# Kernel tuning notes

Hardware: AMD Instinct MI355X
Metric: run time of the kernel (lower is better)

The kernel has to match this reference:

```python
import jax, jax.numpy as jnp
import numpy as np

DIM = 384
NH = 6
HD = DIM // NH  # 64
WS = (6, 12)    # window_size (dilated_size=[1,1] so total_window_size == window_size)
SS = (3, 6)     # shift_size
N = WS[0] * WS[1]  # 72 tokens per window


def _make_mask(H, W):
    # Faithful replication of SD_attn.create_mask (static, so computed in numpy).
    wh, ww = WS
    sh, sw = SS
    img = np.zeros((H, W), np.float32)
    cnt = 0
    for hs in (slice(0, -wh), slice(-wh, -sh), slice(-sh, None)):
        for wsl in (slice(0, -ww), slice(-ww, 0), slice(0, None)):
            img[hs, wsl] = cnt
            cnt += 1
    # window partition -> (nW, N)
    m = img.reshape(H // wh, wh, W // ww, ww).transpose(0, 2, 1, 3).reshape(-1, wh * ww)
    d = m[:, None, :] - m[:, :, None]  # (nW, N, N), [i,j] = m[j]-m[i]
    return np.where(d != 0, -np.inf, 0.0).astype(np.float32)


def _rope2d(x):
    # 2D axial rotary embedding over the (wh, ww) window grid.
    # x: (M, wh, ww, hd); first half of pair-channels rotated by h-position, second half by w-position.
    wh, ww, hd = x.shape[1], x.shape[2], x.shape[3]
    half = hd // 2
    inv = 1.0 / (10000.0 ** (np.arange(0, half, 2, dtype=np.float32) / half))  # (half//2,)
    ah = np.arange(wh, dtype=np.float32)[:, None] * inv  # (wh, half//2)
    aw = np.arange(ww, dtype=np.float32)[:, None] * inv  # (ww, half//2)
    ang = np.concatenate([
        np.broadcast_to(ah[:, None, :], (wh, ww, half // 2)),
        np.broadcast_to(aw[None, :, :], (wh, ww, half // 2)),
    ], -1)  # (wh, ww, half)
    cos = jnp.asarray(np.cos(ang), dtype=x.dtype)
    sin = jnp.asarray(np.sin(ang), dtype=x.dtype)
    x1, x2 = x[..., 0::2], x[..., 1::2]
    return jnp.stack([x1 * cos - x2 * sin, x1 * sin + x2 * cos], -1).reshape(x.shape)


def setup_inputs() -> dict:
    key = jax.random.key(0)
    ks = jax.random.split(key, 5)
    x = jax.random.normal(ks[0], (2, 192, 384, DIM), jnp.float32)
    w_qkv = 0.02 * jax.random.normal(ks[1], (3 * DIM, DIM), jnp.float32)
    b_qkv = 0.02 * jax.random.normal(ks[2], (3 * DIM,), jnp.float32)
    w_proj = 0.02 * jax.random.normal(ks[3], (DIM, DIM), jnp.float32)
    b_proj = 0.02 * jax.random.normal(ks[4], (DIM,), jnp.float32)
    return {"x": x, "w_qkv": w_qkv, "b_qkv": b_qkv, "w_proj": w_proj, "b_proj": b_proj}


def reference(x, w_qkv, b_qkv, w_proj, b_proj):
    B, H, W, C = x.shape
    wh, ww = WS
    sh, sw = SS
    nH, nWc = H // wh, W // ww
    nwin = nH * nWc
    B_ = B * nwin
    scale = HD ** -0.5

    # cyclic shift + window partition (dilated_size=[1,1] => plain swin windows)
    xs = jnp.roll(x, (-sh, -sw), axis=(1, 2))
    xw = xs.reshape(B, nH, wh, nWc, ww, C).transpose(0, 1, 3, 2, 4, 5).reshape(B_, N, C)

    qkv = (xw @ w_qkv.T + b_qkv).reshape(B_, N, 3, NH, HD).transpose(2, 0, 3, 1, 4)
    q, k, v = qkv[0], qkv[1], qkv[2]  # (B_, NH, N, HD)

    q = _rope2d(q.reshape(-1, wh, ww, HD)).reshape(B_, NH, N, HD)
    k = _rope2d(k.reshape(-1, wh, ww, HD)).reshape(B_, NH, N, HD)

    attn = jnp.einsum('bhnd,bhmd->bhnm', q * scale, k)  # (B_, NH, N, N)
    mask = jnp.asarray(_make_mask(H, W))                 # (nwin, N, N)
    attn = (attn.reshape(B, nwin, NH, N, N) + mask[None, :, None]).reshape(B_, NH, N, N)
    attn = jax.nn.softmax(attn, axis=-1)
    save_attn = attn.mean(axis=1)  # mean over heads -> (B_, N, N)

    out = jnp.einsum('bhnm,bhmd->bhnd', attn, v).transpose(0, 2, 1, 3).reshape(B_, N, C)
    out = out.reshape(B, nH, nWc, wh, ww, C).transpose(0, 1, 3, 2, 4, 5).reshape(B, H, W, C)
    out = jnp.roll(out, (sh, sw), axis=(1, 2))
    out = out @ w_proj.T + b_proj
    return out, save_attn
```

## Files before the change

### kernel.cpp

```cpp
#include <hip/hip_runtime.h>

typedef __attribute__((ext_vector_type(8))) __bf16 bf16x8;
typedef __attribute__((ext_vector_type(4))) float f32x4;
typedef unsigned short u16;
typedef unsigned int u32;

__device__ __forceinline__ u16 f2bf(float x){
  u32 u = __float_as_uint(x);
  return (u16)((u + 0x7fffu + ((u >> 16) & 1u)) >> 16);
}
__device__ __forceinline__ u32 pkbf(float lo, float hi){
  u32 r; asm("v_cvt_pk_bf16_f32 %0, %1, %2" : "=v"(r) : "v"(lo), "v"(hi)); return r;
}

union FragU { uint4 u4; bf16x8 bf; };

__device__ __forceinline__ bf16x8 lds_frag(const unsigned char* smem, int off, int row, int strideB, int kElem){
  int byte = (row * strideB + kElem * 2) ^ ((row & 7) << 4);
  FragU f; f.u4 = *reinterpret_cast<const uint4*>(smem + off + byte);
  return f.bf;
}

typedef __attribute__((address_space(3))) unsigned char lds_u8;
typedef __attribute__((address_space(1))) const unsigned char g_u8;
__device__ __forceinline__ void glds16(const void* g, void* l){
  __builtin_amdgcn_global_load_lds((g_u8*)g, (lds_u8*)l, 16, 0, 0);
}

__global__ void prep_weights(const float* __restrict__ wq, const float* __restrict__ wp,
                             u16* __restrict__ wqb, u16* __restrict__ wpb){
  int i = blockIdx.x * 256 + threadIdx.x;
  wqb[i] = f2bf(wq[i]);
  if (i < 147456) wpb[i] = f2bf(wp[i]);
}

__global__ void prep_x(const float* __restrict__ x, u16* __restrict__ xb){
  size_t i = ((size_t)blockIdx.x * 256 + threadIdx.x) * 8;
  float4 f0 = *reinterpret_cast<const float4*>(x + i);
  float4 f1 = *reinterpret_cast<const float4*>(x + i + 4);
  uint4 q;
  q.x = pkbf(f0.x, f0.y); q.y = pkbf(f0.z, f0.w);
  q.z = pkbf(f1.x, f1.y); q.w = pkbf(f1.z, f1.w);
  *reinterpret_cast<uint4*>(xb + i) = q;
}

#define WA_OFF 0
#define WB_OFF 10240
#define WVT    0
#define WTC    61440
#define WTS    62592
__launch_bounds__(256, 2)
__global__ void qkv_win(const u16* __restrict__ xb, const u16* __restrict__ wqb,
                        const float* __restrict__ bq, float* __restrict__ out,
                        u16* __restrict__ vws)
{
  __shared__ __align__(16) unsigned char smem[63744];
  const int tid  = threadIdx.x;
  const int wc   = tid >> 6;
  const int lane = tid & 63;
  const int l15  = lane & 15;
  const int lhi  = lane >> 4;

  const int bid = blockIdx.x;
  const int l   = (bid & 7) * 768 + (bid >> 3);
  const int g   = l / 3;
  const int sec = l - g * 3;
  const int bIdx = g >> 10;
  const int win  = g & 1023;
  const int wi   = win >> 5;
  const int wj   = win & 31;

  auto rowof = [&](int t)->size_t {
    int r = t / 12, c = t - r * 12;
    int hh = wi * 6 + r + 3;  if (hh >= 192) hh -= 192;
    int ww = wj * 12 + c + 6; if (ww >= 384) ww -= 384;
    return ((size_t)bIdx * 192 + hh) * 384 + ww;
  };

  float* tabc = reinterpret_cast<float*>(smem + WTC);
  float* tabs = reinterpret_cast<float*>(smem + WTS);
  for (int i = tid; i < 288; i += 256){
    int pos = i >> 4, m = i & 15;
    float pv = (pos < 6) ? (float)pos : (float)(pos - 6);
    float ang = pv * __expf(-(float)m * 0.5756462732485114f);
    tabc[i] = cosf(ang);
    tabs[i] = sinf(ang);
  }

  size_t arow[3]; int asoff[3]; bool aval[3];
  #pragma unroll
  for (int it = 0; it < 3; ++it){
    int c = it * 256 + tid;
    aval[it] = (it < 2) || (tid < 128);
    int t = c >> 3, p = c & 7;
    int tc = (t < 72) ? t : 71;
    arow[it]  = rowof(tc);
    asoff[it] = ((p ^ (t & 7)) << 3);
  }

  f32x4 acc[5][6];
  #pragma unroll
  for (int mt = 0; mt < 5; ++mt)
    #pragma unroll
    for (int nt = 0; nt < 6; ++nt) acc[mt][nt] = 0.0f;

  for (int kk = 0; kk < 6; ++kk){
    #pragma unroll
    for (int it = 0; it < 3; ++it){
      if (aval[it])
        glds16(xb + arow[it] * 384 + kk * 64 + asoff[it],
               smem + WA_OFF + (it * 256 + tid) * 16);
    }
    #pragma unroll
    for (int it = 0; it < 12; ++it){
      int c = it * 256 + tid;
      int n = c >> 3, p = c & 7;
      glds16(wqb + (size_t)(sec * 384 + n) * 384 + kk * 64 + ((p ^ (n & 7)) << 3),
             smem + WB_OFF + c * 16);
    }
    __syncthreads();
    #pragma unroll
    for (int ks = 0; ks < 2; ++ks){
      const int kEl = ks * 32 + lhi * 8;
      bf16x8 af[5], bfr[6];
      #pragma unroll
      for (int mt = 0; mt < 5; ++mt)
        af[mt] = lds_frag(smem, WA_OFF, mt * 16 + l15, 128, kEl);
      #pragma unroll
      for (int nt = 0; nt < 6; ++nt)
        bfr[nt] = lds_frag(smem, WB_OFF, wc * 96 + nt * 16 + l15, 128, kEl);
      __builtin_amdgcn_s_setprio(1);
      #pragma unroll
      for (int mt = 0; mt < 5; ++mt)
        #pragma unroll
        for (int nt = 0; nt < 6; ++nt)
          acc[mt][nt] = __builtin_amdgcn_mfma_f32_16x16x32_bf16(af[mt], bfr[nt], acc[mt][nt], 0, 0, 0);
      __builtin_amdgcn_s_setprio(0);
    }
    __syncthreads();
  }

  if (sec < 2){
    u16* qk = (u16*)out + (sec ? 56623104u : 0u) + (size_t)g * 27648;
    #pragma unroll
    for (int nt = 0; nt < 6; ++nt){
      const int ch  = wc * 96 + nt * 16 + l15;
      const int h   = ch >> 6;
      const int chh = ch & 63;
      const float bias = bq[sec * 384 + ch];
      const int p2  = chh >> 1;
      const int m   = p2 & 15;
      const bool isR = (p2 < 16);
      const bool ev  = ((chh & 1) == 0);
      #pragma unroll
      for (int mt = 0; mt < 5; ++mt){
        #pragma unroll
        for (int r = 0; r < 4; ++r){
          const int tok = mt * 16 + lhi * 4 + r;
          float v = acc[mt][nt][r] + bias;
          float o = __shfl_xor(v, 1);
          int tr = tok / 12;
          int pos = isR ? tr : (6 + tok - tr * 12);
          float cc = tabc[pos * 16 + m], ssn = tabs[pos * 16 + m];
          float nv = ev ? (v * cc - o * ssn) : (o * ssn + v * cc);
          if (sec == 0) nv *= 0.125f;
          if (tok < 72)
            qk[(size_t)h * 4608 + tok * 64 + chh] = f2bf(nv);
        }
      }
    }
  } else {
    #pragma unroll
    for (int nt = 0; nt < 6; ++nt){
      const int ch = wc * 96 + nt * 16 + l15;
      const float bv = bq[768 + ch];
      #pragma unroll
      for (int mt = 0; mt < 5; ++mt){
        const int tok0 = mt * 16 + lhi * 4;
        uint2 pk;
        pk.x = pkbf(acc[mt][nt][0] + bv, acc[mt][nt][1] + bv);
        pk.y = pkbf(acc[mt][nt][2] + bv, acc[mt][nt][3] + bv);
        *reinterpret_cast<uint2*>(smem + WVT + ch * 160 + tok0 * 2) = pk;
      }
    }
    __syncthreads();
    u16* vd = vws + (size_t)g * 30720;
    #pragma unroll
    for (int it = 0; it < 15; ++it){
      int c  = it * 256 + tid;
      int ch = c / 10;
      int p  = c - ch * 10;
      uint4 val;
      if (p == 9){ val.x = 0; val.y = 0; val.z = 0; val.w = 0; }
      else val = *reinterpret_cast<const uint4*>(smem + WVT + c * 16);
      *reinterpret_cast<uint4*>(vd + (size_t)(ch >> 6) * 5120 + (ch & 63) * 80 + p * 8) = val;
    }
  }
}

#define QH4 0
#define KH4 10240
#define VT4 20480
#define SMEM4 30976
__launch_bounds__(320, 5)
__global__ void win_attn6(const u16* __restrict__ qkg,
                          const u16* __restrict__ vws,
                          float* __restrict__ out,
                          u16* __restrict__ axb)
{
  __shared__ __align__(16) unsigned char smem[SMEM4];
  const int tid  = threadIdx.x;
  const int wave = tid >> 6;
  const int lane = tid & 63;
  const int l15  = lane & 15;
  const int lhi  = lane >> 4;

  const int bid  = blockIdx.x;
  const int wgid = (bid & 7) * 256 + (bid >> 3);
  const int bIdx = wgid >> 10;
  const int win  = wgid & 1023;
  const int wi   = win >> 5;
  const int wj   = win & 31;
  const bool maskWin = (wi == 31);
  const int g    = wgid;

  auto rowof = [&](int t)->size_t {
    int r = t / 12, c = t - r * 12;
    int hh = wi * 6 + r + 3;  if (hh >= 192) hh -= 192;
    int ww = wj * 12 + c + 6; if (ww >= 384) ww -= 384;
    return ((size_t)bIdx * 192 + hh) * 384 + ww;
  };
  const int qtok = wave * 16 + l15;
  const bool tv = (qtok < 72);
  const size_t qrow = rowof(tv ? qtok : 71);

  const u16* qsl0 = qkg + (size_t)g * 27648;
  const u16* ksl0 = qkg + 56623104u + (size_t)g * 27648;
  const u16* vsl0 = vws + (size_t)g * 30720;

  if (tid < 64) *reinterpret_cast<u32*>(smem + VT4 + 10240 + tid * 4) = 0u;

  float sv[5][4];
  #pragma unroll
  for (int a2 = 0; a2 < 5; ++a2)
    #pragma unroll
    for (int b2 = 0; b2 < 4; ++b2) sv[a2][b2] = 0.0f;

  for (int h = 0; h < 6; ++h){
    const u16* qsl = qsl0 + h * 4608;
    const u16* ksl = ksl0 + h * 4608;
    const u16* vsl = vsl0 + h * 5120;
    #pragma unroll
    for (int it = 0; it < 2; ++it){
      int c = it * 320 + tid;
      int t = c >> 3, p = c & 7;
      int tc = (t < 72) ? t : 71;
      int s = (p ^ (t & 7)) << 3;
      glds16(qsl + tc * 64 + s, smem + QH4 + c * 16);
      glds16(ksl + tc * 64 + s, smem + KH4 + c * 16);
      glds16(vsl + c * 8,       smem + VT4 + c * 16);
    }
    __syncthreads();

    f32x4 pf[5];
    #pragma unroll
    for (int nt = 0; nt < 5; ++nt) pf[nt] = 0.0f;
    __builtin_amdgcn_s_setprio(1);
    #pragma unroll
    for (int ks = 0; ks < 2; ++ks){
      const int kEl = ks * 32 + lhi * 8;
      bf16x8 qf = lds_frag(smem, QH4, qtok, 128, kEl);
      #pragma unroll
      for (int nt = 0; nt < 5; ++nt){
        bf16x8 kf = lds_frag(smem, KH4, nt * 16 + l15, 128, kEl);
        pf[nt] = __builtin_amdgcn_mfma_f32_16x16x32_bf16(kf, qf, pf[nt], 0, 0, 0);
      }
    }
    __builtin_amdgcn_s_setprio(0);

    float mx = -1e30f;
    #pragma unroll
    for (int nt = 0; nt < 5; ++nt)
      #pragma unroll
      for (int r = 0; r < 4; ++r){
        const int kk2 = nt * 16 + lhi * 4 + r;
        bool valid = (kk2 < 72) && (!maskWin || ((kk2 < 36) == (qtok < 36)));
        float val = valid ? pf[nt][r] : -1e30f;
        pf[nt][r] = val;
        mx = fmaxf(mx, val);
      }
    mx = fmaxf(mx, __shfl_xor(mx, 16));
    mx = fmaxf(mx, __shfl_xor(mx, 32));
    float sm = 0.0f;
    #pragma unroll
    for (int nt = 0; nt < 5; ++nt)
      #pragma unroll
      for (int r = 0; r < 4; ++r){
        float e = __expf(pf[nt][r] - mx);
        pf[nt][r] = e; sm += e;
      }
    sm += __shfl_xor(sm, 16);
    sm += __shfl_xor(sm, 32);
    const float inv = 1.0f / sm;
    u32 pp[5][2];
    #pragma unroll
    for (int nt = 0; nt < 5; ++nt){
      float p0 = pf[nt][0] * inv, p1 = pf[nt][1] * inv;
      float p2 = pf[nt][2] * inv, p3 = pf[nt][3] * inv;
      sv[nt][0] += p0; sv[nt][1] += p1; sv[nt][2] += p2; sv[nt][3] += p3;
      pp[nt][0] = pkbf(p0, p1);
      pp[nt][1] = pkbf(p2, p3);
    }

    f32x4 oacc[4];
    #pragma unroll
    for (int nt = 0; nt < 4; ++nt) oacc[nt] = 0.0f;
    #pragma unroll
    for (int ks = 0; ks < 3; ++ks){
      FragU pb;
      u32 w[4];
      #pragma unroll
      for (int w_ = 0; w_ < 4; ++w_){
        int srcLane = l15 + 16 * ((lane >> 4 & 1) * 2 + (w_ >> 1));
        u32 c0 = __shfl(pp[ks * 2][w_ & 1], srcLane);
        u32 c1 = (ks * 2 + 1 < 5) ? __shfl(pp[ks * 2 + 1][w_ & 1], srcLane) : 0u;
        w[w_] = (lhi & 2) ? c1 : c0;
      }
      pb.u4.x = w[0]; pb.u4.y = w[1]; pb.u4.z = w[2]; pb.u4.w = w[3];
      const int kEl = ks * 32 + lhi * 8;
      __builtin_amdgcn_s_setprio(1);
      #pragma unroll
      for (int nt = 0; nt < 4; ++nt){
        FragU vf;
        vf.u4 = *reinterpret_cast<const uint4*>(smem + VT4 + (nt * 16 + l15) * 160 + kEl * 2);
        oacc[nt] = __builtin_amdgcn_mfma_f32_16x16x32_bf16(vf.bf, pb.bf, oacc[nt], 0, 0, 0);
      }
      __builtin_amdgcn_s_setprio(0);
    }
    if (tv){
      u16* ao = axb + qrow * 384 + h * 64;
      #pragma unroll
      for (int nt = 0; nt < 4; ++nt){
        uint2 pk;
        pk.x = pkbf(oacc[nt][0], oacc[nt][1]);
        pk.y = pkbf(oacc[nt][2], oacc[nt][3]);
        *reinterpret_cast<uint2*>(ao + nt * 16 + lhi * 4) = pk;
      }
    }
    __syncthreads();
  }

  if (tv){
    float* so = out + 56623104ull + (size_t)wgid * 5184 + (size_t)qtok * 72;
    const float c6 = 1.0f / 6.0f;
    #pragma unroll
    for (int nt = 0; nt < 4; ++nt){
      float4 v4; v4.x = sv[nt][0]*c6; v4.y = sv[nt][1]*c6; v4.z = sv[nt][2]*c6; v4.w = sv[nt][3]*c6;
      *reinterpret_cast<float4*>(so + nt * 16 + lhi * 4) = v4;
    }
    if (lhi < 2){
      float4 v4; v4.x = sv[4][0]*c6; v4.y = sv[4][1]*c6; v4.z = sv[4][2]*c6; v4.w = sv[4][3]*c6;
      *reinterpret_cast<float4*>(so + 64 + lhi * 4) = v4;
    }
  }
}

#define B6STR 12288
__launch_bounds__(512, 4)
__global__ void proj_gemm2(const u16* __restrict__ axb,
                           const u16* __restrict__ wpb, const float* __restrict__ bp,
                           float* __restrict__ out)
{
  __shared__ __align__(16) unsigned char smem[24576];
  const int tid  = threadIdx.x;
  const int wave = tid >> 6;
  const int lane = tid & 63;
  const int l15  = lane & 15;
  const int lhi  = lane >> 4;
  const int wr   = wave >> 2;
  const int wc   = wave & 3;
  const size_t row0 = (size_t)blockIdx.x * 128;
  const int ny   = blockIdx.y;

  const u16* bsec = wpb + (size_t)(ny * 192) * 384;
  auto stageB = [&](int t, int bufOff){
    {
      int c = tid, row = c >> 2, ccd = c & 3;
      int ccs = ccd ^ ((row >> 1) & 3);
      glds16(bsec + (size_t)row * 384 + t * 32 + ccs * 8, smem + bufOff + c * 16);
    }
    if (tid < 256){
      int c = 512 + tid, row = c >> 2, ccd = c & 3;
      int ccs = ccd ^ ((row >> 1) & 3);
      glds16(bsec + (size_t)row * 384 + t * 32 + ccs * 8, smem + bufOff + c * 16);
    }
  };

  const u16* abase = axb + (row0 + wr * 64 + l15) * 384 + lhi * 8;

  f32x4 acc[4][3];
  #pragma unroll
  for (int mt = 0; mt < 4; ++mt)
    #pragma unroll
    for (int nt = 0; nt < 3; ++nt) acc[mt][nt] = 0.0f;

  FragU a_cur[4], a_nxt[4];
  #pragma unroll
  for (int mt = 0; mt < 4; ++mt)
    a_cur[mt].u4 = *reinterpret_cast<const uint4*>(abase + mt * 6144);
  stageB(0, 0);
  __syncthreads();

  int buf = 0;
  for (int t = 0; t < 12; ++t){
    if (t < 11){
      stageB(t + 1, buf ^ B6STR);
      #pragma unroll
      for (int mt = 0; mt < 4; ++mt)
        a_nxt[mt].u4 = *reinterpret_cast<const uint4*>(abase + mt * 6144 + (t + 1) * 32);
    }
    FragU bfr[3];
    #pragma unroll
    for (int nt = 0; nt < 3; ++nt){
      int rown = wc * 48 + nt * 16 + l15;
      int byte = buf + rown * 64 + ((lhi ^ ((rown >> 1) & 3)) << 4);
      bfr[nt].u4 = *reinterpret_cast<const uint4*>(smem + byte);
    }
    #pragma unroll
    for (int mt = 0; mt < 4; ++mt)
      #pragma unroll
      for (int nt = 0; nt < 3; ++nt)
        acc[mt][nt] = __builtin_amdgcn_mfma_f32_16x16x32_bf16(a_cur[mt].bf, bfr[nt].bf, acc[mt][nt], 0, 0, 0);
    __syncthreads();
    #pragma unroll
    for (int mt = 0; mt < 4; ++mt) a_cur[mt] = a_nxt[mt];
    buf ^= B6STR;
  }

  float bpv[3];
  #pragma unroll
  for (int nt = 0; nt < 3; ++nt) bpv[nt] = bp[ny * 192 + wc * 48 + nt * 16 + l15];
  #pragma unroll
  for (int mt = 0; mt < 4; ++mt)
    #pragma unroll
    for (int nt = 0; nt < 3; ++nt){
      const int ch = ny * 192 + wc * 48 + nt * 16 + l15;
      #pragma unroll
      for (int r = 0; r < 4; ++r){
        size_t grow = row0 + wr * 64 + mt * 16 + lhi * 4 + r;
        out[grow * 384 + ch] = acc[mt][nt][r] + bpv[nt];
      }
    }
}

extern "C" void kernel_launch(void* const* d_in, const int* in_sizes, int n_in,
                              void* d_out, int out_size, void* d_ws, size_t ws_size,
                              hipStream_t stream)
{
  const float* x  = (const float*)d_in[0];
  const float* wq = (const float*)d_in[1];
  const float* bq = (const float*)d_in[2];
  const float* wp = (const float*)d_in[3];
  const float* bp = (const float*)d_in[4];
  float* out = (float*)d_out;

  u16* wqb = (u16*)d_ws;
  u16* wpb = (u16*)((char*)d_ws + 442368 * 2);
  u16* vws = (u16*)((char*)d_ws + 1179648);
  u16* xb  = (u16*)((char*)d_ws + 127008768);

  prep_weights<<<1728, 256, 0, stream>>>(wq, wp, wqb, wpb);
  prep_x<<<27648, 256, 0, stream>>>(x, xb);
  qkv_win<<<6144, 256, 0, stream>>>(xb, wqb, bq, out, vws);
  win_attn6<<<2048, 320, 0, stream>>>((const u16*)out, vws, out, xb);
  proj_gemm2<<<dim3(1152, 2), 512, 0, stream>>>(xb, wpb, bp, out);
}
```

Before: 636.3 us.

## Process two windows per QKV block to share weight tiles; swizzle proj grid

The QKV GEMM kernel now uses 512-thread blocks that each handle two adjacent windows. The staged weight tile is shared across both, which halves weight traffic per window and halves the block count. The V writeback is serialized per window through LDS with extra barriers. The projection GEMM switches to a 1D grid with an XCD-aware remap so blocks sharing the same weight half and rows land on the same chiplet. The larger LDS footprint may limit occupancy.

```diff
diff --git a/kernel.cpp b/kernel.cpp
--- a/kernel.cpp
+++ b/kernel.cpp
@@ -44,57 +44,62 @@
   *reinterpret_cast<uint4*>(xb + i) = q;
 }
 
-#define WA_OFF 0
-#define WB_OFF 10240
-#define WVT    0
-#define WTC    61440
-#define WTS    62592
-__launch_bounds__(256, 2)
-__global__ void qkv_win(const u16* __restrict__ xb, const u16* __restrict__ wqb,
-                        const float* __restrict__ bq, float* __restrict__ out,
-                        u16* __restrict__ vws)
+#define W2A  0
+#define W2B  20480
+#define W2VT 0
+#define W2TC 69632
+#define W2TS 70784
+__launch_bounds__(512, 2)
+__global__ void qkv_win2(const u16* __restrict__ xb, const u16* __restrict__ wqb,
+                         const float* __restrict__ bq, float* __restrict__ out,
+                         u16* __restrict__ vws)
 {
-  __shared__ __align__(16) unsigned char smem[63744];
+  __shared__ __align__(16) unsigned char smem[71936];
   const int tid  = threadIdx.x;
-  const int wc   = tid >> 6;
+  const int wave = tid >> 6;
   const int lane = tid & 63;
   const int l15  = lane & 15;
   const int lhi  = lane >> 4;
+  const int wh   = wave >> 2;
+  const int wc   = wave & 3;
 
   const int bid = blockIdx.x;
-  const int l   = (bid & 7) * 768 + (bid >> 3);
-  const int g   = l / 3;
-  const int sec = l - g * 3;
-  const int bIdx = g >> 10;
-  const int win  = g & 1023;
-  const int wi   = win >> 5;
-  const int wj   = win & 31;
-
-  auto rowof = [&](int t)->size_t {
+  const int l   = (bid & 7) * 384 + (bid >> 3);
+  const int g2  = l / 3;
+  const int sec = l - g2 * 3;
+  const int gw  = g2 * 2;
+  const int bIdx = gw >> 10;
+  const int win0 = gw & 1023;
+  const int wi   = win0 >> 5;
+  const int wj0  = win0 & 31;
+
+  auto rowof = [&](int whx, int t)->size_t {
     int r = t / 12, c = t - r * 12;
     int hh = wi * 6 + r + 3;  if (hh >= 192) hh -= 192;
-    int ww = wj * 12 + c + 6; if (ww >= 384) ww -= 384;
+    int ww = (wj0 + whx) * 12 + c + 6; if (ww >= 384) ww -= 384;
     return ((size_t)bIdx * 192 + hh) * 384 + ww;
   };
 
-  float* tabc = reinterpret_cast<float*>(smem + WTC);
-  float* tabs = reinterpret_cast<float*>(smem + WTS);
-  for (int i = tid; i < 288; i += 256){
-    int pos = i >> 4, m = i & 15;
+  float* tabc = reinterpret_cast<float*>(smem + W2TC);
+  float* tabs = reinterpret_cast<float*>(smem + W2TS);
+  if (tid < 288){
+    int pos = tid >> 4, m = tid & 15;
     float pv = (pos < 6) ? (float)pos : (float)(pos - 6);
     float ang = pv * __expf(-(float)m * 0.5756462732485114f);
-    tabc[i] = cosf(ang);
-    tabs[i] = sinf(ang);
-  }
-
-  size_t arow[3]; int asoff[3]; bool aval[3];
+    tabc[tid] = cosf(ang);
+    tabs[tid] = sinf(ang);
+  }
+
+  size_t arow[3]; int asoff[3];
+  const bool aval2 = (tid < 256);
   #pragma unroll
   for (int it = 0; it < 3; ++it){
-    int c = it * 256 + tid;
-    aval[it] = (it < 2) || (tid < 128);
-    int t = c >> 3, p = c & 7;
+    int c = it * 512 + tid;
+    int whx = (c >= 640) ? 1 : 0;
+    int r = c - whx * 640;
+    int t = r >> 3, p = r & 7;
     int tc = (t < 72) ? t : 71;
-    arow[it]  = rowof(tc);
+    arow[it]  = rowof(whx, tc);
     asoff[it] = ((p ^ (t & 7)) << 3);
   }
 
@@ -107,16 +112,16 @@
   for (int kk = 0; kk < 6; ++kk){
     #pragma unroll
     for (int it = 0; it < 3; ++it){
-      if (aval[it])
+      if (it < 2 || aval2)
         glds16(xb + arow[it] * 384 + kk * 64 + asoff[it],
-               smem + WA_OFF + (it * 256 + tid) * 16);
-    }
-    #pragma unroll
-    for (int it = 0; it < 12; ++it){
-      int c = it * 256 + tid;
+               smem + W2A + (it * 512 + tid) * 16);
+    }
+    #pragma unroll
+    for (int it = 0; it < 6; ++it){
+      int c = it * 512 + tid;
       int n = c >> 3, p = c & 7;
       glds16(wqb + (size_t)(sec * 384 + n) * 384 + kk * 64 + ((p ^ (n & 7)) << 3),
-             smem + WB_OFF + c * 16);
+             smem + W2B + c * 16);
     }
     __syncthreads();
     #pragma unroll
@@ -125,10 +130,10 @@
       bf16x8 af[5], bfr[6];
       #pragma unroll
       for (int mt = 0; mt < 5; ++mt)
-        af[mt] = lds_frag(smem, WA_OFF, mt * 16 + l15, 128, kEl);
+        af[mt] = lds_frag(smem, W2A + wh * 10240, mt * 16 + l15, 128, kEl);
       #pragma unroll
       for (int nt = 0; nt < 6; ++nt)
-        bfr[nt] = lds_frag(smem, WB_OFF, wc * 96 + nt * 16 + l15, 128, kEl);
+        bfr[nt] = lds_frag(smem, W2B, wc * 96 + nt * 16 + l15, 128, kEl);
       __builtin_amdgcn_s_setprio(1);
       #pragma unroll
       for (int mt = 0; mt < 5; ++mt)
@@ -141,6 +146,7 @@
   }
 
   if (sec < 2){
+    const int g = gw + wh;
     u16* qk = (u16*)out + (sec ? 56623104u : 0u) + (size_t)g * 27648;
     #pragma unroll
     for (int nt = 0; nt < 6; ++nt){
@@ -171,29 +177,37 @@
     }
   } else {
     #pragma unroll
-    for (int nt = 0; nt < 6; ++nt){
-      const int ch = wc * 96 + nt * 16 + l15;
-      const float bv = bq[768 + ch];
-      #pragma unroll
-      for (int mt = 0; mt < 5; ++mt){
-        const int tok0 = mt * 16 + lhi * 4;
-        uint2 pk;
-        pk.x = pkbf(acc[mt][nt][0] + bv, acc[mt][nt][1] + bv);
-        pk.y = pkbf(acc[mt][nt][2] + bv, acc[mt][nt][3] + bv);
-        *reinterpret_cast<uint2*>(smem + WVT + ch * 160 + tok0 * 2) = pk;
-      }
-    }
-    __syncthreads();
-    u16* vd = vws + (size_t)g * 30720;
-    #pragma unroll
-    for (int it = 0; it < 15; ++it){
-      int c  = it * 256 + tid;
-      int ch = c / 10;
-      int p  = c - ch * 10;
-      uint4 val;
-      if (p == 9){ val.x = 0; val.y = 0; val.z = 0; val.w = 0; }
-      else val = *reinterpret_cast<const uint4*>(smem + WVT + c * 16);
-      *reinterpret_cast<uint4*>(vd + (size_t)(ch >> 6) * 5120 + (ch & 63) * 80 + p * 8) = val;
+    for (int whp = 0; whp < 2; ++whp){
+      if (wh == whp){
+        #pragma unroll
+        for (int nt = 0; nt < 6; ++nt){
+          const int ch = wc * 96 + nt * 16 + l15;
+          const float bv = bq[768 + ch];
+          #pragma unroll
+          for (int mt = 0; mt < 5; ++mt){
+            const int tok0 = mt * 16 + lhi * 4;
+            uint2 pk;
+            pk.x = pkbf(acc[mt][nt][0] + bv, acc[mt][nt][1] + bv);
+            pk.y = pkbf(acc[mt][nt][2] + bv, acc[mt][nt][3] + bv);
+            *reinterpret_cast<uint2*>(smem + W2VT + ch * 160 + tok0 * 2) = pk;
+          }
+        }
+      }
+      __syncthreads();
+      u16* vd = vws + (size_t)(gw + whp) * 30720;
+      #pragma unroll
+      for (int it = 0; it < 8; ++it){
+        int c = it * 512 + tid;
+        if (it < 7 || tid < 256){
+          int ch = c / 10;
+          int p  = c - ch * 10;
+          uint4 val;
+          if (p == 9){ val.x = 0; val.y = 0; val.z = 0; val.w = 0; }
+          else val = *reinterpret_cast<const uint4*>(smem + W2VT + c * 16);
+          *reinterpret_cast<uint4*>(vd + (size_t)(ch >> 6) * 5120 + (ch & 63) * 80 + p * 8) = val;
+        }
+      }
+      __syncthreads();
     }
   }
 }
@@ -379,8 +393,11 @@
   const int lhi  = lane >> 4;
   const int wr   = wave >> 2;
   const int wc   = wave & 3;
-  const size_t row0 = (size_t)blockIdx.x * 128;
-  const int ny   = blockIdx.y;
+
+  const int bid = blockIdx.x;
+  const int l   = (bid & 7) * 288 + (bid >> 3);
+  const size_t row0 = (size_t)(l >> 1) * 128;
+  const int ny  = l & 1;
 
   const u16* bsec = wpb + (size_t)(ny * 192) * 384;
   auto stageB = [&](int t, int bufOff){
@@ -471,7 +488,7 @@
 
   prep_weights<<<1728, 256, 0, stream>>>(wq, wp, wqb, wpb);
   prep_x<<<27648, 256, 0, stream>>>(x, xb);
-  qkv_win<<<6144, 256, 0, stream>>>(xb, wqb, bq, out, vws);
+  qkv_win2<<<3072, 512, 0, stream>>>(xb, wqb, bq, out, vws);
   win_attn6<<<2048, 320, 0, stream>>>((const u16*)out, vws, out, xb);
-  proj_gemm2<<<dim3(1152, 2), 512, 0, stream>>>(xb, wpb, bp, out);
-}
+  proj_gemm2<<<2304, 512, 0, stream>>>(xb, wpb, bp, out);
+}
```

Measured after the change: 647.5 us. Within noise of the previous version (+1.8%).

## Double-buffer per-head LDS staging in window attention and remap projection GEMM blocks

Applied to the files above, without the earlier changes.

The attention kernel now keeps two LDS buffers and prefetches the next head's Q/K/V while computing the current head. This removes one barrier per head and hides global-load latency. The price is doubled LDS use, so occupancy drops from 5 to 3 blocks per CU. The projection GEMM switches to a 1D grid with an XCD-aware block remap, so blocks that share A rows land on the same chiplet's L2.

```diff
diff --git a/kernel.cpp b/kernel.cpp
--- a/kernel.cpp
+++ b/kernel.cpp
@@ -198,17 +198,17 @@
   }
 }
 
-#define QH4 0
-#define KH4 10240
-#define VT4 20480
-#define SMEM4 30976
-__launch_bounds__(320, 5)
-__global__ void win_attn6(const u16* __restrict__ qkg,
+#define AB_Q 0
+#define AB_K 10240
+#define AB_V 20480
+#define AB_SZ 30976
+__launch_bounds__(320, 3)
+__global__ void win_attn7(const u16* __restrict__ qkg,
                           const u16* __restrict__ vws,
                           float* __restrict__ out,
                           u16* __restrict__ axb)
 {
-  __shared__ __align__(16) unsigned char smem[SMEM4];
+  __shared__ __align__(16) unsigned char smem[2 * AB_SZ];
   const int tid  = threadIdx.x;
   const int wave = tid >> 6;
   const int lane = tid & 63;
@@ -238,15 +238,12 @@
   const u16* ksl0 = qkg + 56623104u + (size_t)g * 27648;
   const u16* vsl0 = vws + (size_t)g * 30720;
 
-  if (tid < 64) *reinterpret_cast<u32*>(smem + VT4 + 10240 + tid * 4) = 0u;
-
-  float sv[5][4];
-  #pragma unroll
-  for (int a2 = 0; a2 < 5; ++a2)
-    #pragma unroll
-    for (int b2 = 0; b2 < 4; ++b2) sv[a2][b2] = 0.0f;
-
-  for (int h = 0; h < 6; ++h){
+  if (tid < 64){
+    *reinterpret_cast<u32*>(smem + AB_V + 10240 + tid * 4) = 0u;
+    *reinterpret_cast<u32*>(smem + AB_SZ + AB_V + 10240 + tid * 4) = 0u;
+  }
+
+  auto stage_head = [&](int h, unsigned char* base){
     const u16* qsl = qsl0 + h * 4608;
     const u16* ksl = ksl0 + h * 4608;
     const u16* vsl = vsl0 + h * 5120;
@@ -256,11 +253,24 @@
       int t = c >> 3, p = c & 7;
       int tc = (t < 72) ? t : 71;
       int s = (p ^ (t & 7)) << 3;
-      glds16(qsl + tc * 64 + s, smem + QH4 + c * 16);
-      glds16(ksl + tc * 64 + s, smem + KH4 + c * 16);
-      glds16(vsl + c * 8,       smem + VT4 + c * 16);
-    }
+      glds16(qsl + tc * 64 + s, base + AB_Q + c * 16);
+      glds16(ksl + tc * 64 + s, base + AB_K + c * 16);
+      glds16(vsl + c * 8,       base + AB_V + c * 16);
+    }
+  };
+
+  float sv[5][4];
+  #pragma unroll
+  for (int a2 = 0; a2 < 5; ++a2)
+    #pragma unroll
+    for (int b2 = 0; b2 < 4; ++b2) sv[a2][b2] = 0.0f;
+
+  stage_head(0, smem);
+
+  for (int h = 0; h < 6; ++h){
+    unsigned char* cur = smem + (h & 1) * AB_SZ;
     __syncthreads();
+    if (h < 5) stage_head(h + 1, smem + ((h + 1) & 1) * AB_SZ);
 
     f32x4 pf[5];
     #pragma unroll
@@ -269,10 +279,10 @@
     #pragma unroll
     for (int ks = 0; ks < 2; ++ks){
       const int kEl = ks * 32 + lhi * 8;
-      bf16x8 qf = lds_frag(smem, QH4, qtok, 128, kEl);
+      bf16x8 qf = lds_frag(cur, AB_Q, qtok, 128, kEl);
       #pragma unroll
       for (int nt = 0; nt < 5; ++nt){
-        bf16x8 kf = lds_frag(smem, KH4, nt * 16 + l15, 128, kEl);
+        bf16x8 kf = lds_frag(cur, AB_K, nt * 16 + l15, 128, kEl);
         pf[nt] = __builtin_amdgcn_mfma_f32_16x16x32_bf16(kf, qf, pf[nt], 0, 0, 0);
       }
     }
@@ -332,7 +342,7 @@
       #pragma unroll
       for (int nt = 0; nt < 4; ++nt){
         FragU vf;
-        vf.u4 = *reinterpret_cast<const uint4*>(smem + VT4 + (nt * 16 + l15) * 160 + kEl * 2);
+        vf.u4 = *reinterpret_cast<const uint4*>(cur + AB_V + (nt * 16 + l15) * 160 + kEl * 2);
         oacc[nt] = __builtin_amdgcn_mfma_f32_16x16x32_bf16(vf.bf, pb.bf, oacc[nt], 0, 0, 0);
       }
       __builtin_amdgcn_s_setprio(0);
@@ -347,7 +357,6 @@
         *reinterpret_cast<uint2*>(ao + nt * 16 + lhi * 4) = pk;
       }
     }
-    __syncthreads();
   }
 
   if (tv){
@@ -379,8 +388,11 @@
   const int lhi  = lane >> 4;
   const int wr   = wave >> 2;
   const int wc   = wave & 3;
-  const size_t row0 = (size_t)blockIdx.x * 128;
-  const int ny   = blockIdx.y;
+
+  const int bid = blockIdx.x;
+  const int l   = (bid & 7) * 288 + (bid >> 3);
+  const size_t row0 = (size_t)(l >> 1) * 128;
+  const int ny  = l & 1;
 
   const u16* bsec = wpb + (size_t)(ny * 192) * 384;
   auto stageB = [&](int t, int bufOff){
@@ -472,6 +484,6 @@
   prep_weights<<<1728, 256, 0, stream>>>(wq, wp, wqb, wpb);
   prep_x<<<27648, 256, 0, stream>>>(x, xb);
   qkv_win<<<6144, 256, 0, stream>>>(xb, wqb, bq, out, vws);
-  win_attn6<<<2048, 320, 0, stream>>>((const u16*)out, vws, out, xb);
-  proj_gemm2<<<dim3(1152, 2), 512, 0, stream>>>(xb, wpb, bp, out);
-}
+  win_attn7<<<2048, 320, 0, stream>>>((const u16*)out, vws, out, xb);
+  proj_gemm2<<<2304, 512, 0, stream>>>(xb, wpb, bp, out);
+}
```

After: 644.1 us. About the same (+1.2%).

## Fuse QKV projection and window attention into one kernel keeping QKV in LDS

Applied to the files above, without the earlier changes.

Merges the QKV GEMM and window-attention kernels into one per-window kernel. It stages the window's full input rows in shared memory once, then loops over heads: a double-buffered weight slice feeds the Q/K/V GEMM, RoPE is applied, and Q/K/V are written to LDS instead of global memory before attention. This removes the global write and re-read of the Q/K/V intermediates and one kernel launch. The cost is about 140KB of shared memory per block, which limits each CU to one 4-wave block, and the QKV weights are re-streamed per window. The projection GEMM grid is also flattened with an XCD-aware block remap.

```diff
diff --git a/kernel.cpp b/kernel.cpp
--- a/kernel.cpp
+++ b/kernel.cpp
@@ -44,31 +44,33 @@
   *reinterpret_cast<uint4*>(xb + i) = q;
 }
 
-#define WA_OFF 0
-#define WB_OFF 10240
-#define WVT    0
-#define WTC    61440
-#define WTS    62592
-__launch_bounds__(256, 2)
-__global__ void qkv_win(const u16* __restrict__ xb, const u16* __restrict__ wqb,
-                        const float* __restrict__ bq, float* __restrict__ out,
-                        u16* __restrict__ vws)
+#define FA   0
+#define FB   61440
+#define FBS  24576
+#define FQ   110592
+#define FK   120832
+#define FV   131072
+#define FTC  141568
+#define FTS  142720
+__launch_bounds__(256, 1)
+__global__ void fused_win(const u16* __restrict__ xb, const u16* __restrict__ wqb,
+                          const float* __restrict__ bq, float* __restrict__ out,
+                          u16* __restrict__ axb)
 {
-  __shared__ __align__(16) unsigned char smem[63744];
+  __shared__ __align__(16) unsigned char smem[143872];
   const int tid  = threadIdx.x;
-  const int wc   = tid >> 6;
+  const int wave = tid >> 6;
   const int lane = tid & 63;
   const int l15  = lane & 15;
   const int lhi  = lane >> 4;
 
-  const int bid = blockIdx.x;
-  const int l   = (bid & 7) * 768 + (bid >> 3);
-  const int g   = l / 3;
-  const int sec = l - g * 3;
+  const int bid  = blockIdx.x;
+  const int g    = (bid & 7) * 256 + (bid >> 3);
   const int bIdx = g >> 10;
   const int win  = g & 1023;
   const int wi   = win >> 5;
   const int wj   = win & 31;
+  const bool maskWin = (wi == 31);
 
   auto rowof = [&](int t)->size_t {
     int r = t / 12, c = t - r * 12;
@@ -77,8 +79,8 @@
     return ((size_t)bIdx * 192 + hh) * 384 + ww;
   };
 
-  float* tabc = reinterpret_cast<float*>(smem + WTC);
-  float* tabs = reinterpret_cast<float*>(smem + WTS);
+  float* tabc = reinterpret_cast<float*>(smem + FTC);
+  float* tabs = reinterpret_cast<float*>(smem + FTS);
   for (int i = tid; i < 288; i += 256){
     int pos = i >> 4, m = i & 15;
     float pv = (pos < 6) ? (float)pos : (float)(pos - 6);
@@ -86,281 +88,233 @@
     tabc[i] = cosf(ang);
     tabs[i] = sinf(ang);
   }
-
-  size_t arow[3]; int asoff[3]; bool aval[3];
-  #pragma unroll
-  for (int it = 0; it < 3; ++it){
-    int c = it * 256 + tid;
-    aval[it] = (it < 2) || (tid < 128);
-    int t = c >> 3, p = c & 7;
-    int tc = (t < 72) ? t : 71;
-    arow[it]  = rowof(tc);
-    asoff[it] = ((p ^ (t & 7)) << 3);
+  if (tid < 64) *reinterpret_cast<u32*>(smem + FV + 10240 + tid * 4) = 0u;
+
+  #pragma unroll
+  for (int it = 0; it < 15; ++it){
+    int c   = it * 256 + tid;
+    int row = c / 48;
+    int p   = c - row * 48;
+    int tc  = (row < 72) ? row : 71;
+    int s   = (p & ~7) | ((p & 7) ^ (row & 7));
+    glds16(xb + rowof(tc) * 384 + s * 8, smem + FA + c * 16);
   }
 
-  f32x4 acc[5][6];
-  #pragma unroll
-  for (int mt = 0; mt < 5; ++mt)
-    #pragma unroll
-    for (int nt = 0; nt < 6; ++nt) acc[mt][nt] = 0.0f;
-
-  for (int kk = 0; kk < 6; ++kk){
-    #pragma unroll
-    for (int it = 0; it < 3; ++it){
-      if (aval[it])
-        glds16(xb + arow[it] * 384 + kk * 64 + asoff[it],
-               smem + WA_OFF + (it * 256 + tid) * 16);
-    }
-    #pragma unroll
-    for (int it = 0; it < 12; ++it){
+  auto stageB = [&](int h, int kk, int bufOff){
+    #pragma unroll
+    for (int it = 0; it < 6; ++it){
       int c = it * 256 + tid;
       int n = c >> 3, p = c & 7;
-      glds16(wqb + (size_t)(sec * 384 + n) * 384 + kk * 64 + ((p ^ (n & 7)) << 3),
-             smem + WB_OFF + c * 16);
+      size_t wrow = (size_t)((n >> 6) * 384 + h * 64 + (n & 63));
+      glds16(wqb + wrow * 384 + kk * 64 + ((p ^ (n & 7)) << 3),
+             smem + bufOff + c * 16);
+    }
+  };
+
+  stageB(0, 0, FB);
+  __syncthreads();
+
+  float sv[2][5][4];
+  #pragma unroll
+  for (int qi = 0; qi < 2; ++qi)
+    #pragma unroll
+    for (int a2 = 0; a2 < 5; ++a2)
+      #pragma unroll
+      for (int b2 = 0; b2 < 4; ++b2) sv[qi][a2][b2] = 0.0f;
+
+  int cur = 0;
+  for (int h = 0; h < 6; ++h){
+    f32x4 acc[5][3];
+    #pragma unroll
+    for (int mt = 0; mt < 5; ++mt)
+      #pragma unroll
+      for (int nt = 0; nt < 3; ++nt) acc[mt][nt] = 0.0f;
+
+    for (int kk = 0; kk < 6; ++kk){
+      if (kk < 5) stageB(h, kk + 1, FB + (cur ^ 1) * FBS);
+      #pragma unroll
+      for (int ks = 0; ks < 2; ++ks){
+        const int kEl = kk * 64 + ks * 32 + lhi * 8;
+        const int bEl = ks * 32 + lhi * 8;
+        bf16x8 afr[5], bfr[3];
+        #pragma unroll
+        for (int mt = 0; mt < 5; ++mt)
+          afr[mt] = lds_frag(smem, FA, mt * 16 + l15, 768, kEl);
+        #pragma unroll
+        for (int nt = 0; nt < 3; ++nt)
+          bfr[nt] = lds_frag(smem, FB + cur * FBS, wave * 48 + nt * 16 + l15, 128, bEl);
+        __builtin_amdgcn_s_setprio(1);
+        #pragma unroll
+        for (int mt = 0; mt < 5; ++mt)
+          #pragma unroll
+          for (int nt = 0; nt < 3; ++nt)
+            acc[mt][nt] = __builtin_amdgcn_mfma_f32_16x16x32_bf16(afr[mt], bfr[nt], acc[mt][nt], 0, 0, 0);
+        __builtin_amdgcn_s_setprio(0);
+      }
+      __syncthreads();
+      if (kk < 5) cur ^= 1;
+    }
+
+    #pragma unroll
+    for (int nt = 0; nt < 3; ++nt){
+      const int ch  = wave * 48 + nt * 16 + l15;
+      const int sec = ch >> 6;
+      const int chh = ch & 63;
+      const float bias = bq[sec * 384 + h * 64 + chh];
+      if (sec < 2){
+        const int p2 = chh >> 1;
+        const int m  = p2 & 15;
+        const bool isR = (p2 < 16);
+        const bool ev  = ((chh & 1) == 0);
+        const int dstOff = sec ? FK : FQ;
+        #pragma unroll
+        for (int mt = 0; mt < 5; ++mt){
+          #pragma unroll
+          for (int r = 0; r < 4; ++r){
+            const int tok = mt * 16 + lhi * 4 + r;
+            float v = acc[mt][nt][r] + bias;
+            float o = __shfl_xor(v, 1);
+            int tr = tok / 12;
+            int pos = isR ? tr : (6 + tok - tr * 12);
+            float cc = tabc[pos * 16 + m], ssn = tabs[pos * 16 + m];
+            float nv = ev ? (v * cc - o * ssn) : (o * ssn + v * cc);
+            if (sec == 0) nv *= 0.125f;
+            int byte = (tok * 128 + chh * 2) ^ ((tok & 7) << 4);
+            *reinterpret_cast<u16*>(smem + dstOff + byte) = f2bf(nv);
+          }
+        }
+      } else {
+        #pragma unroll
+        for (int mt = 0; mt < 5; ++mt){
+          const int tok0 = mt * 16 + lhi * 4;
+          uint2 pk;
+          pk.x = pkbf(acc[mt][nt][0] + bias, acc[mt][nt][1] + bias);
+          pk.y = pkbf(acc[mt][nt][2] + bias, acc[mt][nt][3] + bias);
+          *reinterpret_cast<uint2*>(smem + FV + chh * 160 + tok0 * 2) = pk;
+        }
+      }
     }
     __syncthreads();
-    #pragma unroll
-    for (int ks = 0; ks < 2; ++ks){
-      const int kEl = ks * 32 + lhi * 8;
-      bf16x8 af[5], bfr[6];
-      #pragma unroll
-      for (int mt = 0; mt < 5; ++mt)
-        af[mt] = lds_frag(smem, WA_OFF, mt * 16 + l15, 128, kEl);
-      #pragma unroll
-      for (int nt = 0; nt < 6; ++nt)
-        bfr[nt] = lds_frag(smem, WB_OFF, wc * 96 + nt * 16 + l15, 128, kEl);
+
+    if (h < 5) stageB(h + 1, 0, FB + (cur ^ 1) * FBS);
+
+    const int nqi = (wave == 3) ? 2 : 1;
+    for (int qi = 0; qi < nqi; ++qi){
+      const int qt   = qi ? 4 : wave;
+      const int qtok = qt * 16 + l15;
+      const bool tv  = (qtok < 72);
+
+      f32x4 pf[5];
+      #pragma unroll
+      for (int nt = 0; nt < 5; ++nt) pf[nt] = 0.0f;
       __builtin_amdgcn_s_setprio(1);
       #pragma unroll
-      for (int mt = 0; mt < 5; ++mt)
-        #pragma unroll
-        for (int nt = 0; nt < 6; ++nt)
-          acc[mt][nt] = __builtin_amdgcn_mfma_f32_16x16x32_bf16(af[mt], bfr[nt], acc[mt][nt], 0, 0, 0);
+      for (int ks = 0; ks < 2; ++ks){
+        const int kEl = ks * 32 + lhi * 8;
+        bf16x8 qf = lds_frag(smem, FQ, qtok, 128, kEl);
+        #pragma unroll
+        for (int nt = 0; nt < 5; ++nt){
+          bf16x8 kf = lds_frag(smem, FK, nt * 16 + l15, 128, kEl);
+          pf[nt] = __builtin_amdgcn_mfma_f32_16x16x32_bf16(kf, qf, pf[nt], 0, 0, 0);
+        }
+      }
       __builtin_amdgcn_s_setprio(0);
+
+      float mx = -1e30f;
+      #pragma unroll
+      for (int nt = 0; nt < 5; ++nt)
+        #pragma unroll
+        for (int r = 0; r < 4; ++r){
+          const int kk2 = nt * 16 + lhi * 4 + r;
+          bool valid = (kk2 < 72) && (!maskWin || ((kk2 < 36) == (qtok < 36)));
+          float val = valid ? pf[nt][r] : -1e30f;
+          pf[nt][r] = val;
+          mx = fmaxf(mx, val);
+        }
+      mx = fmaxf(mx, __shfl_xor(mx, 16));
+      mx = fmaxf(mx, __shfl_xor(mx, 32));
+      float sm = 0.0f;
+      #pragma unroll
+      for (int nt = 0; nt < 5; ++nt)
+        #pragma unroll
+        for (int r = 0; r < 4; ++r){
+          float e = __expf(pf[nt][r] - mx);
+          pf[nt][r] = e; sm += e;
+        }
+      sm += __shfl_xor(sm, 16);
+      sm += __shfl_xor(sm, 32);
+      const float inv = 1.0f / sm;
+      u32 pp[5][2];
+      #pragma unroll
+      for (int nt = 0; nt < 5; ++nt){
+        float p0 = pf[nt][0] * inv, p1 = pf[nt][1] * inv;
+        float p2 = pf[nt][2] * inv, p3 = pf[nt][3] * inv;
+        sv[qi][nt][0] += p0; sv[qi][nt][1] += p1;
+        sv[qi][nt][2] += p2; sv[qi][nt][3] += p3;
+        pp[nt][0] = pkbf(p0, p1);
+        pp[nt][1] = pkbf(p2, p3);
+      }
+
+      f32x4 oacc[4];
+      #pragma unroll
+      for (int nt = 0; nt < 4; ++nt) oacc[nt] = 0.0f;
+      #pragma unroll
+      for (int ks = 0; ks < 3; ++ks){
+        FragU pb;
+        u32 w[4];
+        #pragma unroll
+        for (int w_ = 0; w_ < 4; ++w_){
+          int srcLane = l15 + 16 * ((lane >> 4 & 1) * 2 + (w_ >> 1));
+          u32 c0 = __shfl(pp[ks * 2][w_ & 1], srcLane);
+          u32 c1 = (ks * 2 + 1 < 5) ? __shfl(pp[ks * 2 + 1][w_ & 1], srcLane) : 0u;
+          w[w_] = (lhi & 2) ? c1 : c0;
+        }
+        pb.u4.x = w[0]; pb.u4.y = w[1]; pb.u4.z = w[2]; pb.u4.w = w[3];
+        const int kEl = ks * 32 + lhi * 8;
+        __builtin_amdgcn_s_setprio(1);
+        #pragma unroll
+        for (int nt = 0; nt < 4; ++nt){
+          FragU vf;
+          vf.u4 = *reinterpret_cast<const uint4*>(smem + FV + (nt * 16 + l15) * 160 + kEl * 2);
+          oacc[nt] = __builtin_amdgcn_mfma_f32_16x16x32_bf16(vf.bf, pb.bf, oacc[nt], 0, 0, 0);
+        }
+        __builtin_amdgcn_s_setprio(0);
+      }
+      if (tv){
+        u16* ao = axb + rowof(qtok) * 384 + h * 64;
+        #pragma unroll
+        for (int nt = 0; nt < 4; ++nt){
+          uint2 pk;
+          pk.x = pkbf(oacc[nt][0], oacc[nt][1]);
+          pk.y = pkbf(oacc[nt][2], oacc[nt][3]);
+          *reinterpret_cast<uint2*>(ao + nt * 16 + lhi * 4) = pk;
+        }
+      }
     }
     __syncthreads();
+    if (h < 5) cur ^= 1;
   }
 
-  if (sec < 2){
-    u16* qk = (u16*)out + (sec ? 56623104u : 0u) + (size_t)g * 27648;
-    #pragma unroll
-    for (int nt = 0; nt < 6; ++nt){
-      const int ch  = wc * 96 + nt * 16 + l15;
-      const int h   = ch >> 6;
-      const int chh = ch & 63;
-      const float bias = bq[sec * 384 + ch];
-      const int p2  = chh >> 1;
-      const int m   = p2 & 15;
-      const bool isR = (p2 < 16);
-      const bool ev  = ((chh & 1) == 0);
-      #pragma unroll
-      for (int mt = 0; mt < 5; ++mt){
-        #pragma unroll
-        for (int r = 0; r < 4; ++r){
-          const int tok = mt * 16 + lhi * 4 + r;
-          float v = acc[mt][nt][r] + bias;
-          float o = __shfl_xor(v, 1);
-          int tr = tok / 12;
-          int pos = isR ? tr : (6 + tok - tr * 12);
-          float cc = tabc[pos * 16 + m], ssn = tabs[pos * 16 + m];
-          float nv = ev ? (v * cc - o * ssn) : (o * ssn + v * cc);
-          if (sec == 0) nv *= 0.125f;
-          if (tok < 72)
-            qk[(size_t)h * 4608 + tok * 64 + chh] = f2bf(nv);
-        }
-      }
-    }
-  } else {
-    #pragma unroll
-    for (int nt = 0; nt < 6; ++nt){
-      const int ch = wc * 96 + nt * 16 + l15;
-      const float bv = bq[768 + ch];
-      #pragma unroll
-      for (int mt = 0; mt < 5; ++mt){
-        const int tok0 = mt * 16 + lhi * 4;
-        uint2 pk;
-        pk.x = pkbf(acc[mt][nt][0] + bv, acc[mt][nt][1] + bv);
-        pk.y = pkbf(acc[mt][nt][2] + bv, acc[mt][nt][3] + bv);
-        *reinterpret_cast<uint2*>(smem + WVT + ch * 160 + tok0 * 2) = pk;
-      }
-    }
-    __syncthreads();
-    u16* vd = vws + (size_t)g * 30720;
-    #pragma unroll
-    for (int it = 0; it < 15; ++it){
-      int c  = it * 256 + tid;
-      int ch = c / 10;
-      int p  = c - ch * 10;
-      uint4 val;
-      if (p == 9){ val.x = 0; val.y = 0; val.z = 0; val.w = 0; }
-      else val = *reinterpret_cast<const uint4*>(smem + WVT + c * 16);
-      *reinterpret_cast<uint4*>(vd + (size_t)(ch >> 6) * 5120 + (ch & 63) * 80 + p * 8) = val;
-    }
-  }
-}
-
-#define QH4 0
-#define KH4 10240
-#define VT4 20480
-#define SMEM4 30976
-__launch_bounds__(320, 5)
-__global__ void win_attn6(const u16* __restrict__ qkg,
-                          const u16* __restrict__ vws,
-                          float* __restrict__ out,
-                          u16* __restrict__ axb)
-{
-  __shared__ __align__(16) unsigned char smem[SMEM4];
-  const int tid  = threadIdx.x;
-  const int wave = tid >> 6;
-  const int lane = tid & 63;
-  const int l15  = lane & 15;
-  const int lhi  = lane >> 4;
-
-  const int bid  = blockIdx.x;
-  const int wgid = (bid & 7) * 256 + (bid >> 3);
-  const int bIdx = wgid >> 10;
-  const int win  = wgid & 1023;
-  const int wi   = win >> 5;
-  const int wj   = win & 31;
-  const bool maskWin = (wi == 31);
-  const int g    = wgid;
-
-  auto rowof = [&](int t)->size_t {
-    int r = t / 12, c = t - r * 12;
-    int hh = wi * 6 + r + 3;  if (hh >= 192) hh -= 192;
-    int ww = wj * 12 + c + 6; if (ww >= 384) ww -= 384;
-    return ((size_t)bIdx * 192 + hh) * 384 + ww;
-  };
-  const int qtok = wave * 16 + l15;
-  const bool tv = (qtok < 72);
-  const size_t qrow = rowof(tv ? qtok : 71);
-
-  const u16* qsl0 = qkg + (size_t)g * 27648;
-  const u16* ksl0 = qkg + 56623104u + (size_t)g * 27648;
-  const u16* vsl0 = vws + (size_t)g * 30720;
-
-  if (tid < 64) *reinterpret_cast<u32*>(smem + VT4 + 10240 + tid * 4) = 0u;
-
-  float sv[5][4];
-  #pragma unroll
-  for (int a2 = 0; a2 < 5; ++a2)
-    #pragma unroll
-    for (int b2 = 0; b2 < 4; ++b2) sv[a2][b2] = 0.0f;
-
-  for (int h = 0; h < 6; ++h){
-    const u16* qsl = qsl0 + h * 4608;
-    const u16* ksl = ksl0 + h * 4608;
-    const u16* vsl = vsl0 + h * 5120;
-    #pragma unroll
-    for (int it = 0; it < 2; ++it){
-      int c = it * 320 + tid;
-      int t = c >> 3, p = c & 7;
-      int tc = (t < 72) ? t : 71;
-      int s = (p ^ (t & 7)) << 3;
-      glds16(qsl + tc * 64 + s, smem + QH4 + c * 16);
-      glds16(ksl + tc * 64 + s, smem + KH4 + c * 16);
-      glds16(vsl + c * 8,       smem + VT4 + c * 16);
-    }
-    __syncthreads();
-
-    f32x4 pf[5];
-    #pragma unroll
-    for (int nt = 0; nt < 5; ++nt) pf[nt] = 0.0f;
-    __builtin_amdgcn_s_setprio(1);
-    #pragma unroll
-    for (int ks = 0; ks < 2; ++ks){
-      const int kEl = ks * 32 + lhi * 8;
-      bf16x8 qf = lds_frag(smem, QH4, qtok, 128, kEl);
-      #pragma unroll
-      for (int nt = 0; nt < 5; ++nt){
-        bf16x8 kf = lds_frag(smem, KH4, nt * 16 + l15, 128, kEl);
-        pf[nt] = __builtin_amdgcn_mfma_f32_16x16x32_bf16(kf, qf, pf[nt], 0, 0, 0);
-      }
-    }
-    __builtin_amdgcn_s_setprio(0);
-
-    float mx = -1e30f;
-    #pragma unroll
-    for (int nt = 0; nt < 5; ++nt)
-      #pragma unroll
-      for (int r = 0; r < 4; ++r){
-        const int kk2 = nt * 16 + lhi * 4 + r;
-        bool valid = (kk2 < 72) && (!maskWin || ((kk2 < 36) == (qtok < 36)));
-        float val = valid ? pf[nt][r] : -1e30f;
-        pf[nt][r] = val;
-        mx = fmaxf(mx, val);
-      }
-    mx = fmaxf(mx, __shfl_xor(mx, 16));
-    mx = fmaxf(mx, __shfl_xor(mx, 32));
-    float sm = 0.0f;
-    #pragma unroll
-    for (int nt = 0; nt < 5; ++nt)
-      #pragma unroll
-      for (int r = 0; r < 4; ++r){
-        float e = __expf(pf[nt][r] - mx);
-        pf[nt][r] = e; sm += e;
-      }
-    sm += __shfl_xor(sm, 16);
-    sm += __shfl_xor(sm, 32);
-    const float inv = 1.0f / sm;
-    u32 pp[5][2];
-    #pragma unroll
-    for (int nt = 0; nt < 5; ++nt){
-      float p0 = pf[nt][0] * inv, p1 = pf[nt][1] * inv;
-      float p2 = pf[nt][2] * inv, p3 = pf[nt][3] * inv;
-      sv[nt][0] += p0; sv[nt][1] += p1; sv[nt][2] += p2; sv[nt][3] += p3;
-      pp[nt][0] = pkbf(p0, p1);
-      pp[nt][1] = pkbf(p2, p3);
-    }
-
-    f32x4 oacc[4];
-    #pragma unroll
-    for (int nt = 0; nt < 4; ++nt) oacc[nt] = 0.0f;
-    #pragma unroll
-    for (int ks = 0; ks < 3; ++ks){
-      FragU pb;
-      u32 w[4];
-      #pragma unroll
-      for (int w_ = 0; w_ < 4; ++w_){
-        int srcLane = l15 + 16 * ((lane >> 4 & 1) * 2 + (w_ >> 1));
-        u32 c0 = __shfl(pp[ks * 2][w_ & 1], srcLane);
-        u32 c1 = (ks * 2 + 1 < 5) ? __shfl(pp[ks * 2 + 1][w_ & 1], srcLane) : 0u;
-        w[w_] = (lhi & 2) ? c1 : c0;
-      }
-      pb.u4.x = w[0]; pb.u4.y = w[1]; pb.u4.z = w[2]; pb.u4.w = w[3];
-      const int kEl = ks * 32 + lhi * 8;
-      __builtin_amdgcn_s_setprio(1);
+  const int nqi = (wave == 3) ? 2 : 1;
+  for (int qi = 0; qi < nqi; ++qi){
+    const int qt   = qi ? 4 : wave;
+    const int qtok = qt * 16 + l15;
+    if (qtok < 72){
+      float* so = out + 56623104ull + (size_t)g * 5184 + (size_t)qtok * 72;
+      const float c6 = 1.0f / 6.0f;
       #pragma unroll
       for (int nt = 0; nt < 4; ++nt){
-        FragU vf;
-        vf.u4 = *reinterpret_cast<const uint4*>(smem + VT4 + (nt * 16 + l15) * 160 + kEl * 2);
-        oacc[nt] = __builtin_amdgcn_mfma_f32_16x16x32_bf16(vf.bf, pb.bf, oacc[nt], 0, 0, 0);
-      }
-      __builtin_amdgcn_s_setprio(0);
-    }
-    if (tv){
-      u16* ao = axb + qrow * 384 + h * 64;
-      #pragma unroll
-      for (int nt = 0; nt < 4; ++nt){
-        uint2 pk;
-        pk.x = pkbf(oacc[nt][0], oacc[nt][1]);
-        pk.y = pkbf(oacc[nt][2], oacc[nt][3]);
-        *reinterpret_cast<uint2*>(ao + nt * 16 + lhi * 4) = pk;
-      }
-    }
-    __syncthreads();
-  }
-
-  if (tv){
-    float* so = out + 56623104ull + (size_t)wgid * 5184 + (size_t)qtok * 72;
-    const float c6 = 1.0f / 6.0f;
-    #pragma unroll
-    for (int nt = 0; nt < 4; ++nt){
-      float4 v4; v4.x = sv[nt][0]*c6; v4.y = sv[nt][1]*c6; v4.z = sv[nt][2]*c6; v4.w = sv[nt][3]*c6;
-      *reinterpret_cast<float4*>(so + nt * 16 + lhi * 4) = v4;
-    }
-    if (lhi < 2){
-      float4 v4; v4.x = sv[4][0]*c6; v4.y = sv[4][1]*c6; v4.z = sv[4][2]*c6; v4.w = sv[4][3]*c6;
-      *reinterpret_cast<float4*>(so + 64 + lhi * 4) = v4;
+        float4 v4;
+        v4.x = sv[qi][nt][0]*c6; v4.y = sv[qi][nt][1]*c6;
+        v4.z = sv[qi][nt][2]*c6; v4.w = sv[qi][nt][3]*c6;
+        *reinterpret_cast<float4*>(so + nt * 16 + lhi * 4) = v4;
+      }
+      if (lhi < 2){
+        float4 v4;
+        v4.x = sv[qi][4][0]*c6; v4.y = sv[qi][4][1]*c6;
+        v4.z = sv[qi][4][2]*c6; v4.w = sv[qi][4][3]*c6;
+        *reinterpret_cast<float4*>(so + 64 + lhi * 4) = v4;
+      }
     }
   }
 }
@@ -379,8 +333,11 @@
   const int lhi  = lane >> 4;
   const int wr   = wave >> 2;
   const int wc   = wave & 3;
-  const size_t row0 = (size_t)blockIdx.x * 128;
-  const int ny   = blockIdx.y;
+
+  const int bid = blockIdx.x;
+  const int l   = (bid & 7) * 288 + (bid >> 3);
+  const size_t row0 = (size_t)(l >> 1) * 128;
+  const int ny  = l & 1;
 
   const u16* bsec = wpb + (size_t)(ny * 192) * 384;
   auto stageB = [&](int t, int bufOff){
@@ -466,12 +423,10 @@
 
   u16* wqb = (u16*)d_ws;
   u16* wpb = (u16*)((char*)d_ws + 442368 * 2);
-  u16* vws = (u16*)((char*)d_ws + 1179648);
   u16* xb  = (u16*)((char*)d_ws + 127008768);
 
   prep_weights<<<1728, 256, 0, stream>>>(wq, wp, wqb, wpb);
   prep_x<<<27648, 256, 0, stream>>>(x, xb);
-  qkv_win<<<6144, 256, 0, stream>>>(xb, wqb, bq, out, vws);
-  win_attn6<<<2048, 320, 0, stream>>>((const u16*)out, vws, out, xb);
-  proj_gemm2<<<dim3(1152, 2), 512, 0, stream>>>(xb, wpb, bp, out);
-}
+  fused_win<<<2048, 256, 0, stream>>>(xb, wqb, bq, out, xb);
+  proj_gemm2<<<2304, 512, 0, stream>>>(xb, wpb, bp, out);
+}
```

New measurement: 810.6 us. 1.27x slower.
